# Kernel optimization log

Measured on AMD Instinct MI355X. Metric: run time of the kernel, lower is better.

Reference implementation:

```python
import jax, jax.numpy as jnp
import numpy as np
import math


def _align_seq_len(e, target_n):
    # e: (B, H, N_enc, hd) -> (B, H, target_n, hd) via bilinear resize on sqrt grid
    B, H, N_enc, D = e.shape
    if N_enc == target_n:
        return e
    h_e = int(math.sqrt(N_enc))
    h_t = int(math.sqrt(target_n))
    img = jnp.transpose(e, (0, 1, 3, 2)).reshape(B, H, D, h_e, h_e)
    img = jax.image.resize(img, (B, H, D, h_t, h_t), method='bilinear')
    return jnp.transpose(img.reshape(B, H, D, target_n), (0, 1, 3, 2))


def setup_inputs() -> dict:
    key = jax.random.key(0)
    ks = jax.random.split(key, 7)
    B, N, D, H = 4, 1024, 1152, 16
    hd = D // H
    N_enc = 1024
    s_in = 1.0 / math.sqrt(D)
    return {
        'x': jax.random.normal(ks[0], (B, N, D), jnp.float32),
        'enc_k': jax.random.normal(ks[1], (B, H, N_enc, hd), jnp.float32),
        'enc_v': jax.random.normal(ks[2], (B, H, N_enc, hd), jnp.float32),
        'qkv_w': jax.random.normal(ks[3], (3 * D, D), jnp.float32) * s_in,
        'qkv_b': jax.random.normal(ks[4], (3 * D,), jnp.float32) * 0.02,
        'proj_w': jax.random.normal(ks[5], (D, D), jnp.float32) * s_in,
        'proj_b': jax.random.normal(ks[6], (D,), jnp.float32) * 0.02,
        'stage': 2,
    }


def reference(x, enc_k, enc_v, qkv_w, qkv_b, proj_w, proj_b, stage):
    B, N, C = x.shape
    H = enc_k.shape[1]
    hd = C // H
    scale = hd ** (-0.5)

    qkv = (x @ qkv_w.T + qkv_b).reshape(B, N, 3, H, hd)
    qkv = jnp.transpose(qkv, (2, 0, 3, 1, 4))  # (3, B, H, N, hd)
    q, k, v = qkv[0], qkv[1], qkv[2]

    distill_loss = jnp.float32(0.0)
    if stage == 1:
        ek = _align_seq_len(enc_k, N)
        ev = _align_seq_len(enc_v, N)
        attn = jax.nn.softmax(jnp.einsum('bhnd,bhmd->bhnm', q * scale, ek), axis=-1)
        x_out = jnp.einsum('bhnm,bhmd->bhnd', attn, ev)
    elif stage == 2:
        ek = _align_seq_len(enc_k, N)
        ev = _align_seq_len(enc_v, N)
        attn_own = jax.nn.softmax(jnp.einsum('bhnd,bhmd->bhnm', q * scale, k), axis=-1)
        x_out = jnp.einsum('bhnm,bhmd->bhnd', attn_own, v)
        qd = jax.lax.stop_gradient(q)
        attn_enc = jax.nn.softmax(jnp.einsum('bhnd,bhmd->bhnm', qd * scale, ek), axis=-1)
        o_star = jax.lax.stop_gradient(jnp.einsum('bhnm,bhmd->bhnd', attn_enc, ev))
        distill_loss = jnp.mean((x_out - o_star) ** 2)
    else:
        attn = jax.nn.softmax(jnp.einsum('bhnd,bhmd->bhnm', q * scale, k), axis=-1)
        x_out = jnp.einsum('bhnm,bhmd->bhnd', attn, v)

    x_out = jnp.transpose(x_out, (0, 2, 1, 3)).reshape(B, N, C)
    out = x_out @ proj_w.T + proj_b
    return out, distill_loss
```

## Files before the change

kernel.cpp:

```cpp
#include <hip/hip_runtime.h>
#include <hip/hip_bf16.h>

#define PB 4
#define PN 1024
#define PC 1152
#define PH 16
#define PHD 72
#define BH 64
#define QKV_COLS 3456
#define OUT_ELEMS ((size_t)PB*PN*PC)
#define K_DIM 1152

#define CHUNK_HALVES 6144
#define HEAD_HALVES (16*CHUNK_HALVES)
#define BUF_HALVES ((size_t)BH*HEAD_HALVES)

typedef _Float16 half8_t __attribute__((ext_vector_type(8)));
typedef _Float16 half4_t __attribute__((ext_vector_type(4)));
typedef float float4v __attribute__((ext_vector_type(4)));

#define QSCALE (0.11785113019775792f * 1.4426950408889634f)

__device__ __forceinline__ void load16_lds(const _Float16* g, _Float16* l) {
    __builtin_amdgcn_global_load_lds(
        (const __attribute__((address_space(1))) void*)g,
        (__attribute__((address_space(3))) void*)l, 16, 0, 0);
}

__device__ __forceinline__ half8_t cvt8(const float* p) {
    float4 a = *(const float4*)p;
    float4 b = *(const float4*)(p + 4);
    half8_t h;
    h[0] = (_Float16)a.x; h[1] = (_Float16)a.y; h[2] = (_Float16)a.z; h[3] = (_Float16)a.w;
    h[4] = (_Float16)b.x; h[5] = (_Float16)b.y; h[6] = (_Float16)b.z; h[7] = (_Float16)b.w;
    return h;
}

#define S0 589824
#define S1 1087488
#define S2 1253376
#define S3 1449984
#define S4 1843200
#define S5 1859584
#define S6 1859585
#define S7 2449409
#define S8 3039233

__global__ __launch_bounds__(256) void prep_all(
    const float* __restrict__ x, const float* __restrict__ qkv_w,
    const float* __restrict__ proj_w,
    const float* __restrict__ ek, const float* __restrict__ ev,
    _Float16* __restrict__ xh, _Float16* __restrict__ qkvwh,
    _Float16* __restrict__ projwh,
    _Float16* __restrict__ qh, _Float16* __restrict__ kh, _Float16* __restrict__ ekh,
    _Float16* __restrict__ vth, _Float16* __restrict__ evth,
    float* __restrict__ loss_out)
{
    int i = blockIdx.x * 256 + threadIdx.x;
    if (i >= S8) return;

    if (i < S0) {
        ((half8_t*)xh)[i] = cvt8(x + (size_t)i * 8);
    } else if (i < S1) {
        int j = i - S0;
        ((half8_t*)qkvwh)[j] = cvt8(qkv_w + (size_t)j * 8);
    } else if (i < S2) {
        int j = i - S1;
        ((half8_t*)projwh)[j] = cvt8(proj_w + (size_t)j * 8);
    } else if (i < S3) {
        int j = i - S2;
        int chunk = j / 192, within = j - chunk * 192;
        half8_t h = {};
        if (within < 64) h[0] = (_Float16)(-4.0f);
        *(half8_t*)(qh + (size_t)chunk * CHUNK_HALVES + 4608 + within * 8) = h;
    } else if (i < S4) {
        int j = i - S3;
        _Float16* base = (j < 196608) ? kh : ekh;
        int jj = (j < 196608) ? j : j - 196608;
        int chunk = jj / 192, within = jj - chunk * 192;
        half8_t h = {};
        if (within < 64) h[0] = (_Float16)1.0f;
        *(half8_t*)(base + (size_t)chunk * CHUNK_HALVES + 4608 + within * 8) = h;
    } else if (i < S5) {
        int j = i - S4;
        _Float16* base = (j < 8192) ? vth : evth;
        int jj = j & 8191;
        int chunk = jj >> 3, kq = jj & 7;
        half8_t o;
#pragma unroll
        for (int r = 0; r < 8; ++r) o[r] = (_Float16)1.0f;
        *(half8_t*)&base[(size_t)chunk * CHUNK_HALVES + kq * 768 + 576] = o;
    } else if (i < S6) {
        *loss_out = 0.0f;
    } else if (i < S7) {
        int j = i - S6;
        int bh = j / 9216, r2 = j - bh * 9216;
        int nblk = r2 / 576, ii = r2 - nblk * 576;
        int n = ii / 9, dq = ii - n * 9;
        const float* s = ek + ((size_t)bh * PN + nblk * 64 + n) * PHD + dq * 8;
        _Float16* kd = ekh + ((size_t)bh * 16 + nblk) * CHUNK_HALVES;
        *(half8_t*)&kd[dq * 512 + n * 8] = cvt8(s);
    } else {
        int j = i - S7;
        int bh = j / 9216, r2 = j - bh * 9216;
        int nblk = r2 / 576, ii = r2 - nblk * 576;
        int nq = ii / 72, d = ii - nq * 72;
        const float* vs = ev + ((size_t)bh * PN + nblk * 64) * PHD;
        _Float16* vd = evth + ((size_t)bh * 16 + nblk) * CHUNK_HALVES;
        half8_t h;
#pragma unroll
        for (int r = 0; r < 8; ++r)
            h[r] = (_Float16)vs[(nq * 8 + r) * PHD + d];
        *(half8_t*)&vd[nq * 768 + d * 8] = h;
    }
}

template<int MODE>
__global__ __launch_bounds__(256) void gemm_mfma(
    const _Float16* __restrict__ A, const _Float16* __restrict__ Bm,
    const float* __restrict__ bias,
    _Float16* __restrict__ qh, _Float16* __restrict__ kh,
    _Float16* __restrict__ vth, float* __restrict__ out, int c_tiles)
{
    const int t    = threadIdx.x;
    const int lane = t & 63;
    const int w    = t >> 6;
    const int wm   = w >> 1, wn = w & 1;
    const int lrow = lane & 15, quad = lane >> 4;

    const int cpx = gridDim.x >> 3;
    const int bid = blockIdx.x;
    const int wg  = (bid & 7) * cpx + (bid >> 3);

    const int per_group = c_tiles * 8;
    const int g  = wg / per_group;
    const int r_ = wg - g * per_group;
    const int m0 = (g * 8 + (r_ & 7)) * 128;
    const int c0 = (r_ >> 3) * 128;

    const bool tr = (MODE == 1) || (c0 < 2 * PC);

    __shared__ _Float16 As[8192];
    __shared__ _Float16 Bs[8192];

    int rowS[4], koff[4], ldsOff[4];
#pragma unroll
    for (int i = 0; i < 4; ++i) {
        int idx = w * 256 + i * 64 + lane;
        int kt2 = idx >> 9, qq = (idx >> 7) & 3;
        rowS[i]   = idx & 127;
        koff[i]   = kt2 * 32 + qq * 8;
        ldsOff[i] = idx * 8;
    }

    const _Float16* aBase = A  + (size_t)m0 * K_DIM;
    const _Float16* bBase = Bm + (size_t)c0 * K_DIM;

    float4v acc[4][4];
#pragma unroll
    for (int ti = 0; ti < 4; ++ti)
#pragma unroll
        for (int tj = 0; tj < 4; ++tj)
            acc[ti][tj] = (float4v){0.f, 0.f, 0.f, 0.f};

    for (int kb = 0; kb < K_DIM; kb += 64) {
        __syncthreads();
#pragma unroll
        for (int i = 0; i < 4; ++i) {
            load16_lds(aBase + (size_t)rowS[i] * K_DIM + kb + koff[i], &As[ldsOff[i]]);
            load16_lds(bBase + (size_t)rowS[i] * K_DIM + kb + koff[i], &Bs[ldsOff[i]]);
        }
        __syncthreads();
#pragma unroll
        for (int s = 0; s < 2; ++s) {
            half8_t af[4], bf[4];
#pragma unroll
            for (int ti = 0; ti < 4; ++ti)
                af[ti] = *(const half8_t*)&As[(((s * 4 + quad) * 128) + wm * 64 + ti * 16 + lrow) * 8];
#pragma unroll
            for (int tj = 0; tj < 4; ++tj)
                bf[tj] = *(const half8_t*)&Bs[(((s * 4 + quad) * 128) + wn * 64 + tj * 16 + lrow) * 8];
            if (tr) {
#pragma unroll
                for (int ti = 0; ti < 4; ++ti)
#pragma unroll
                    for (int tj = 0; tj < 4; ++tj)
                        acc[ti][tj] = __builtin_amdgcn_mfma_f32_16x16x32_f16(
                            bf[tj], af[ti], acc[ti][tj], 0, 0, 0);
            } else {
#pragma unroll
                for (int ti = 0; ti < 4; ++ti)
#pragma unroll
                    for (int tj = 0; tj < 4; ++tj)
                        acc[ti][tj] = __builtin_amdgcn_mfma_f32_16x16x32_f16(
                            af[ti], bf[tj], acc[ti][tj], 0, 0, 0);
            }
        }
    }

    if (MODE == 1) {
#pragma unroll
        for (int tj = 0; tj < 4; ++tj) {
            int cg = c0 + wn * 64 + tj * 16 + quad * 4;
            float4v bv = *(const float4v*)&bias[cg];
#pragma unroll
            for (int ti = 0; ti < 4; ++ti) {
                int m = m0 + wm * 64 + ti * 16 + lrow;
                float4v o;
#pragma unroll
                for (int r = 0; r < 4; ++r) o[r] = acc[ti][tj][r] + bv[r];
                *(float4v*)&out[(size_t)m * PC + cg] = o;
            }
        }
    } else if (tr) {
        const int jq = c0 / PC;
        const float mulv = (jq == 0) ? QSCALE : 1.f;
        _Float16* dstp = (jq == 0) ? qh : kh;
#pragma unroll
        for (int tj = 0; tj < 4; ++tj) {
            int cg  = c0 + wn * 64 + tj * 16 + quad * 4;
            int rem = cg - jq * PC;
            int h   = rem / PHD;
            int ds  = rem - h * PHD;
            float4v bv = *(const float4v*)&bias[cg];
#pragma unroll
            for (int ti = 0; ti < 4; ++ti) {
                int m = m0 + wm * 64 + ti * 16 + lrow;
                int b = m >> 10, n = m & 1023;
                size_t chunk = ((size_t)(b * PH + h) * 16 + (n >> 6)) * CHUNK_HALVES;
                half4_t hv;
#pragma unroll
                for (int r = 0; r < 4; ++r)
                    hv[r] = (_Float16)((acc[ti][tj][r] + bv[r]) * mulv);
                *(half4_t*)&dstp[chunk + (ds >> 3) * 512 + (n & 63) * 8 + (ds & 7)] = hv;
            }
        }
    } else {
#pragma unroll
        for (int tj = 0; tj < 4; ++tj) {
            int c   = c0 + wn * 64 + tj * 16 + lrow;
            int rem = c - 2 * PC;
            int h   = rem / PHD;
            int d   = rem - h * PHD;
            float bv = bias[c];
#pragma unroll
            for (int ti = 0; ti < 4; ++ti) {
                int mg = m0 + wm * 64 + ti * 16 + quad * 4;
                int b = mg >> 10, n = mg & 1023;
                size_t chunk = ((size_t)(b * PH + h) * 16 + (n >> 6)) * CHUNK_HALVES;
                half4_t hv;
#pragma unroll
                for (int r = 0; r < 4; ++r)
                    hv[r] = (_Float16)(acc[ti][tj][r] + bv);
                *(half4_t*)&vth[chunk + ((n & 63) >> 3) * 768 + d * 8 + (n & 7)] = hv;
            }
        }
    }
}

__device__ __forceinline__ void attn_step(
    const half8_t* qf, const _Float16* Ks, const _Float16* Vts, _Float16* Pw,
    float4v* O, int ln, int quad)
{
    float4v accS[4];
#pragma unroll
    for (int ct = 0; ct < 4; ++ct) accS[ct] = (float4v){0.f, 0.f, 0.f, 0.f};
    __builtin_amdgcn_s_setprio(1);
#pragma unroll
    for (int ks = 0; ks < 3; ++ks) {
#pragma unroll
        for (int ct = 0; ct < 4; ++ct) {
            half8_t kf = *(const half8_t*)&Ks[(((ks * 4 + quad) * 64) + ct * 16 + ln) * 8];
            accS[ct] = __builtin_amdgcn_mfma_f32_16x16x32_f16(kf, qf[ks], accS[ct], 0, 0, 0);
        }
    }
    __builtin_amdgcn_s_setprio(0);

    const int pbase = (quad >> 1) * 128 + ln * 8 + (quad & 1) * 4;
#pragma unroll
    for (int ct = 0; ct < 4; ++ct) {
        half4_t pk;
#pragma unroll
        for (int r = 0; r < 4; ++r)
            pk[r] = (_Float16)exp2f(accS[ct][r]);
        *(half4_t*)&Pw[pbase + ct * 256] = pk;
    }

    __builtin_amdgcn_s_setprio(1);
#pragma unroll
    for (int ks = 0; ks < 2; ++ks) {
        half8_t pf = *(const half8_t*)&Pw[(ks * 4 + quad) * 128 + ln * 8];
#pragma unroll
        for (int ct = 0; ct < 5; ++ct) {
            half8_t vf = *(const half8_t*)&Vts[(((ks * 4 + quad) * 96) + ct * 16 + ln) * 8];
            O[ct] = __builtin_amdgcn_mfma_f32_16x16x32_f16(vf, pf, O[ct], 0, 0, 0);
        }
    }
    __builtin_amdgcn_s_setprio(0);
}

__global__ __launch_bounds__(256, 4) void attn_fused(
    const _Float16* __restrict__ qh, const _Float16* __restrict__ kh,
    const _Float16* __restrict__ vth,
    const _Float16* __restrict__ ekh, const _Float16* __restrict__ evth,
    _Float16* __restrict__ xouth, float* __restrict__ loss_out)
{
    const int t = threadIdx.x;
    const int lane = t & 63;
    const int w = t >> 6;
    const int ln = lane & 15;
    const int quad = lane >> 4;

    const int lid  = blockIdx.x;
    const int bh   = (lid & 7) * 8 + ((lid >> 3) >> 4);
    const int nblk = (lid >> 3) & 15;

    __shared__ _Float16 Ks[CHUNK_HALVES];
    __shared__ _Float16 Vs[CHUNK_HALVES];
    __shared__ _Float16 Ps[4096];
    __shared__ float red[256];

    _Float16* Pw = Ps + w * 1024;

    const _Float16* qc = qh + ((size_t)bh * 16 + nblk) * CHUNK_HALVES;
    half8_t qf[3];
#pragma unroll
    for (int ks = 0; ks < 3; ++ks)
        qf[ks] = *(const half8_t*)&qc[(((ks * 4 + quad) * 64) + w * 16 + ln) * 8];

    const _Float16* kbo = kh   + (size_t)bh * HEAD_HALVES;
    const _Float16* vbo = vth  + (size_t)bh * HEAD_HALVES;
    const _Float16* kbe = ekh  + (size_t)bh * HEAD_HALVES;
    const _Float16* vbe = evth + (size_t)bh * HEAD_HALVES;

    float4v Oo[5], Oe[5];
#pragma unroll
    for (int ct = 0; ct < 5; ++ct) {
        Oo[ct] = (float4v){0.f, 0.f, 0.f, 0.f};
        Oe[ct] = (float4v){0.f, 0.f, 0.f, 0.f};
    }

    for (int kt = 0; kt < 16; ++kt) {
        const _Float16* kc = kbo + (size_t)kt * CHUNK_HALVES;
        const _Float16* vc = vbo + (size_t)kt * CHUNK_HALVES;
        __syncthreads();
#pragma unroll
        for (int i = 0; i < 3; ++i) {
            int u = i * 256 + t;
            load16_lds(kc + u * 8, &Ks[u * 8]);
            load16_lds(vc + u * 8, &Vs[u * 8]);
        }
        __syncthreads();
        attn_step(qf, Ks, Vs, Pw, Oo, ln, quad);
    }
    for (int kt = 0; kt < 16; ++kt) {
        const _Float16* kc = kbe + (size_t)kt * CHUNK_HALVES;
        const _Float16* vc = vbe + (size_t)kt * CHUNK_HALVES;
        __syncthreads();
#pragma unroll
        for (int i = 0; i < 3; ++i) {
            int u = i * 256 + t;
            load16_lds(kc + u * 8, &Ks[u * 8]);
            load16_lds(vc + u * 8, &Vs[u * 8]);
        }
        __syncthreads();
        attn_step(qf, Ks, Vs, Pw, Oe, ln, quad);
    }

    float l_o = __shfl(Oo[4][0], 32 + ln);
    float l_e = __shfl(Oe[4][0], 32 + ln);
    const float inv_o = 1.0f / l_o;
    const float inv_e = 1.0f / l_e;

    const int b = bh >> 4, h = bh & 15;
    const int nrow = nblk * 64 + w * 16 + ln;

    float lacc = 0.f;
    const size_t rowbase = (size_t)(b * PN + nrow) * PC + h * PHD;
#pragma unroll
    for (int ct = 0; ct < 5; ++ct) {
        int d0 = ct * 16 + quad * 4;
        if (d0 < PHD) {
            half4_t oh;
#pragma unroll
            for (int r = 0; r < 4; ++r) {
                float own = Oo[ct][r] * inv_o;
                oh[r] = (_Float16)own;
                float df = own - Oe[ct][r] * inv_e;
                lacc += df * df;
            }
            *(half4_t*)&xouth[rowbase + d0] = oh;
        }
    }

    red[t] = lacc;
    __syncthreads();
    for (int off = 128; off > 0; off >>= 1) {
        if (t < off) red[t] += red[t + off];
        __syncthreads();
    }
    if (t == 0) atomicAdd(loss_out, red[0] * (1.0f / (float)OUT_ELEMS));
}

extern "C" void kernel_launch(void* const* d_in, const int* in_sizes, int n_in,
                              void* d_out, int out_size, void* d_ws, size_t ws_size,
                              hipStream_t stream)
{
    const float* x      = (const float*)d_in[0];
    const float* enc_k  = (const float*)d_in[1];
    const float* enc_v  = (const float*)d_in[2];
    const float* qkv_w  = (const float*)d_in[3];
    const float* qkv_b  = (const float*)d_in[4];
    const float* proj_w = (const float*)d_in[5];
    const float* proj_b = (const float*)d_in[6];

    float* out = (float*)d_out;

    _Float16* x_h     = (_Float16*)d_ws;
    _Float16* qkvw_h  = x_h + OUT_ELEMS;
    _Float16* projw_h = qkvw_h + (size_t)QKV_COLS * PC;
    _Float16* xout_h  = projw_h + (size_t)PC * PC;
    _Float16* q_h     = xout_h + OUT_ELEMS;
    _Float16* k_h     = q_h  + BUF_HALVES;
    _Float16* vt_h    = k_h  + BUF_HALVES;
    _Float16* ek_h    = vt_h + BUF_HALVES;
    _Float16* evt_h   = ek_h + BUF_HALVES;

    prep_all<<<11873, 256, 0, stream>>>(
        x, qkv_w, proj_w, enc_k, enc_v,
        x_h, qkvw_h, projw_h, q_h, k_h, ek_h, vt_h, evt_h, out + OUT_ELEMS);

    gemm_mfma<0><<<(QKV_COLS / 128) * ((PB * PN) / 128), 256, 0, stream>>>(
        x_h, qkvw_h, qkv_b, q_h, k_h, vt_h, nullptr, QKV_COLS / 128);

    attn_fused<<<16 * BH, 256, 0, stream>>>(
        q_h, k_h, vt_h, ek_h, evt_h, xout_h, out + OUT_ELEMS);

    gemm_mfma<1><<<(PC / 128) * ((PB * PN) / 128), 256, 0, stream>>>(
        xout_h, projw_h, proj_b, nullptr, nullptr, nullptr, out, PC / 128);
}
```

Baseline: 308.9 us.

## Process two query blocks per attention workgroup to reuse K/V tiles

```diff
diff --git a/kernel.cpp b/kernel.cpp
--- a/kernel.cpp
+++ b/kernel.cpp
@@ -258,48 +258,55 @@
     }
 }
 
-__device__ __forceinline__ void attn_step(
-    const half8_t* qf, const _Float16* Ks, const _Float16* Vts, _Float16* Pw,
-    float4v* O, int ln, int quad)
+__device__ __forceinline__ void attn_step2(
+    const half8_t* qfA, const half8_t* qfB,
+    const _Float16* Ks, const _Float16* Vts,
+    _Float16* PwA, _Float16* PwB,
+    float4v* OA, float4v* OB, int ln, int quad)
 {
-    float4v accS[4];
-#pragma unroll
-    for (int ct = 0; ct < 4; ++ct) accS[ct] = (float4v){0.f, 0.f, 0.f, 0.f};
-    __builtin_amdgcn_s_setprio(1);
+    float4v sA[4], sB[4];
+#pragma unroll
+    for (int ct = 0; ct < 4; ++ct) {
+        sA[ct] = (float4v){0.f, 0.f, 0.f, 0.f};
+        sB[ct] = (float4v){0.f, 0.f, 0.f, 0.f};
+    }
 #pragma unroll
     for (int ks = 0; ks < 3; ++ks) {
 #pragma unroll
         for (int ct = 0; ct < 4; ++ct) {
             half8_t kf = *(const half8_t*)&Ks[(((ks * 4 + quad) * 64) + ct * 16 + ln) * 8];
-            accS[ct] = __builtin_amdgcn_mfma_f32_16x16x32_f16(kf, qf[ks], accS[ct], 0, 0, 0);
-        }
-    }
-    __builtin_amdgcn_s_setprio(0);
+            sA[ct] = __builtin_amdgcn_mfma_f32_16x16x32_f16(kf, qfA[ks], sA[ct], 0, 0, 0);
+            sB[ct] = __builtin_amdgcn_mfma_f32_16x16x32_f16(kf, qfB[ks], sB[ct], 0, 0, 0);
+        }
+    }
 
     const int pbase = (quad >> 1) * 128 + ln * 8 + (quad & 1) * 4;
 #pragma unroll
     for (int ct = 0; ct < 4; ++ct) {
-        half4_t pk;
-#pragma unroll
-        for (int r = 0; r < 4; ++r)
-            pk[r] = (_Float16)exp2f(accS[ct][r]);
-        *(half4_t*)&Pw[pbase + ct * 256] = pk;
-    }
-
-    __builtin_amdgcn_s_setprio(1);
+        half4_t pkA, pkB;
+#pragma unroll
+        for (int r = 0; r < 4; ++r) {
+            pkA[r] = (_Float16)exp2f(sA[ct][r]);
+            pkB[r] = (_Float16)exp2f(sB[ct][r]);
+        }
+        *(half4_t*)&PwA[pbase + ct * 256] = pkA;
+        *(half4_t*)&PwB[pbase + ct * 256] = pkB;
+    }
+
 #pragma unroll
     for (int ks = 0; ks < 2; ++ks) {
-        half8_t pf = *(const half8_t*)&Pw[(ks * 4 + quad) * 128 + ln * 8];
+        half8_t pfA = *(const half8_t*)&PwA[(ks * 4 + quad) * 128 + ln * 8];
+        half8_t pfB = *(const half8_t*)&PwB[(ks * 4 + quad) * 128 + ln * 8];
 #pragma unroll
         for (int ct = 0; ct < 5; ++ct) {
             half8_t vf = *(const half8_t*)&Vts[(((ks * 4 + quad) * 96) + ct * 16 + ln) * 8];
-            O[ct] = __builtin_amdgcn_mfma_f32_16x16x32_f16(vf, pf, O[ct], 0, 0, 0);
-        }
-    }
-    __builtin_amdgcn_s_setprio(0);
-}
-
-__global__ __launch_bounds__(256, 4) void attn_fused(
+            OA[ct] = __builtin_amdgcn_mfma_f32_16x16x32_f16(vf, pfA, OA[ct], 0, 0, 0);
+            OB[ct] = __builtin_amdgcn_mfma_f32_16x16x32_f16(vf, pfB, OB[ct], 0, 0, 0);
+        }
+    }
+}
+
+__global__ __launch_bounds__(256, 2) void attn_fused(
     const _Float16* __restrict__ qh, const _Float16* __restrict__ kh,
     const _Float16* __restrict__ vth,
     const _Float16* __restrict__ ekh, const _Float16* __restrict__ evth,
@@ -311,33 +318,37 @@
     const int ln = lane & 15;
     const int quad = lane >> 4;
 
-    const int lid  = blockIdx.x;
-    const int bh   = (lid & 7) * 8 + ((lid >> 3) >> 4);
-    const int nblk = (lid >> 3) & 15;
+    const int lid   = blockIdx.x;
+    const int bh    = (lid & 7) * 8 + (lid >> 6);
+    const int npair = (lid >> 3) & 7;
 
     __shared__ _Float16 Ks[CHUNK_HALVES];
     __shared__ _Float16 Vs[CHUNK_HALVES];
-    __shared__ _Float16 Ps[4096];
-    __shared__ float red[256];
-
-    _Float16* Pw = Ps + w * 1024;
-
-    const _Float16* qc = qh + ((size_t)bh * 16 + nblk) * CHUNK_HALVES;
-    half8_t qf[3];
-#pragma unroll
-    for (int ks = 0; ks < 3; ++ks)
-        qf[ks] = *(const half8_t*)&qc[(((ks * 4 + quad) * 64) + w * 16 + ln) * 8];
+    __shared__ _Float16 Ps[16384 / 2];
+    float* red = (float*)Ps;
+
+    _Float16* PwA = Ps + w * 2048;
+    _Float16* PwB = PwA + 1024;
+
+    const _Float16* qcA = qh + ((size_t)bh * 16 + npair * 2) * CHUNK_HALVES;
+    const _Float16* qcB = qcA + CHUNK_HALVES;
+    half8_t qfA[3], qfB[3];
+#pragma unroll
+    for (int ks = 0; ks < 3; ++ks) {
+        qfA[ks] = *(const half8_t*)&qcA[(((ks * 4 + quad) * 64) + w * 16 + ln) * 8];
+        qfB[ks] = *(const half8_t*)&qcB[(((ks * 4 + quad) * 64) + w * 16 + ln) * 8];
+    }
 
     const _Float16* kbo = kh   + (size_t)bh * HEAD_HALVES;
     const _Float16* vbo = vth  + (size_t)bh * HEAD_HALVES;
     const _Float16* kbe = ekh  + (size_t)bh * HEAD_HALVES;
     const _Float16* vbe = evth + (size_t)bh * HEAD_HALVES;
 
-    float4v Oo[5], Oe[5];
+    float4v OoA[5], OoB[5];
 #pragma unroll
     for (int ct = 0; ct < 5; ++ct) {
-        Oo[ct] = (float4v){0.f, 0.f, 0.f, 0.f};
-        Oe[ct] = (float4v){0.f, 0.f, 0.f, 0.f};
+        OoA[ct] = (float4v){0.f, 0.f, 0.f, 0.f};
+        OoB[ct] = (float4v){0.f, 0.f, 0.f, 0.f};
     }
 
     for (int kt = 0; kt < 16; ++kt) {
@@ -351,8 +362,16 @@
             load16_lds(vc + u * 8, &Vs[u * 8]);
         }
         __syncthreads();
-        attn_step(qf, Ks, Vs, Pw, Oo, ln, quad);
-    }
+        attn_step2(qfA, qfB, Ks, Vs, PwA, PwB, OoA, OoB, ln, quad);
+    }
+
+    float4v OeA[5], OeB[5];
+#pragma unroll
+    for (int ct = 0; ct < 5; ++ct) {
+        OeA[ct] = (float4v){0.f, 0.f, 0.f, 0.f};
+        OeB[ct] = (float4v){0.f, 0.f, 0.f, 0.f};
+    }
+
     for (int kt = 0; kt < 16; ++kt) {
         const _Float16* kc = kbe + (size_t)kt * CHUNK_HALVES;
         const _Float16* vc = vbe + (size_t)kt * CHUNK_HALVES;
@@ -364,35 +383,42 @@
             load16_lds(vc + u * 8, &Vs[u * 8]);
         }
         __syncthreads();
-        attn_step(qf, Ks, Vs, Pw, Oe, ln, quad);
-    }
-
-    float l_o = __shfl(Oo[4][0], 32 + ln);
-    float l_e = __shfl(Oe[4][0], 32 + ln);
-    const float inv_o = 1.0f / l_o;
-    const float inv_e = 1.0f / l_e;
+        attn_step2(qfA, qfB, Ks, Vs, PwA, PwB, OeA, OeB, ln, quad);
+    }
+
+    const float inv_oA = 1.0f / __shfl(OoA[4][0], 32 + ln);
+    const float inv_oB = 1.0f / __shfl(OoB[4][0], 32 + ln);
+    const float inv_eA = 1.0f / __shfl(OeA[4][0], 32 + ln);
+    const float inv_eB = 1.0f / __shfl(OeB[4][0], 32 + ln);
 
     const int b = bh >> 4, h = bh & 15;
-    const int nrow = nblk * 64 + w * 16 + ln;
+    const int nrowA = npair * 128 + w * 16 + ln;
+    const int nrowB = nrowA + 64;
 
     float lacc = 0.f;
-    const size_t rowbase = (size_t)(b * PN + nrow) * PC + h * PHD;
+    const size_t rbA = (size_t)(b * PN + nrowA) * PC + h * PHD;
+    const size_t rbB = (size_t)(b * PN + nrowB) * PC + h * PHD;
 #pragma unroll
     for (int ct = 0; ct < 5; ++ct) {
         int d0 = ct * 16 + quad * 4;
         if (d0 < PHD) {
-            half4_t oh;
+            half4_t ohA, ohB;
 #pragma unroll
             for (int r = 0; r < 4; ++r) {
-                float own = Oo[ct][r] * inv_o;
-                oh[r] = (_Float16)own;
-                float df = own - Oe[ct][r] * inv_e;
-                lacc += df * df;
+                float ownA = OoA[ct][r] * inv_oA;
+                float ownB = OoB[ct][r] * inv_oB;
+                ohA[r] = (_Float16)ownA;
+                ohB[r] = (_Float16)ownB;
+                float dA = ownA - OeA[ct][r] * inv_eA;
+                float dB = ownB - OeB[ct][r] * inv_eB;
+                lacc += dA * dA + dB * dB;
             }
-            *(half4_t*)&xouth[rowbase + d0] = oh;
-        }
-    }
-
+            *(half4_t*)&xouth[rbA + d0] = ohA;
+            *(half4_t*)&xouth[rbB + d0] = ohB;
+        }
+    }
+
+    __syncthreads();
     red[t] = lacc;
     __syncthreads();
     for (int off = 128; off > 0; off >>= 1) {
@@ -433,7 +459,7 @@
     gemm_mfma<0><<<(QKV_COLS / 128) * ((PB * PN) / 128), 256, 0, stream>>>(
         x_h, qkvw_h, qkv_b, q_h, k_h, vt_h, nullptr, QKV_COLS / 128);
 
-    attn_fused<<<16 * BH, 256, 0, stream>>>(
+    attn_fused<<<512, 256, 0, stream>>>(
         q_h, k_h, vt_h, ek_h, evt_h, xout_h, out + OUT_ELEMS);
 
     gemm_mfma<1><<<(PC / 128) * ((PB * PN) / 128), 256, 0, stream>>>(
```

Result: no change. 307.6 us (-0.4%).
